# Optimization experiments

Measured on AMD Instinct MI355X. Metric: run time of the kernel, lower is better.

## Reference

```python
import jax, jax.numpy as jnp
import numpy as np

EMB = 1024
HEADS = 16
HEAD_DIM = EMB // HEADS
B, T = 2, 2048
EPS = 1e-5


def setup_inputs() -> dict:
    key = jax.random.key(0)
    ks = jax.random.split(key, 12)
    s_in = (1.0 / np.sqrt(EMB)).astype(np.float32)
    s_hid = (1.0 / np.sqrt(4 * EMB)).astype(np.float32)
    return {
        "x": jax.random.normal(ks[0], (B, T, EMB), jnp.float32),
        "Wq": jax.random.normal(ks[1], (HEADS, EMB, HEAD_DIM), jnp.float32) * s_in,
        "Wk": jax.random.normal(ks[2], (HEADS, EMB, HEAD_DIM), jnp.float32) * s_in,
        "Wv": jax.random.normal(ks[3], (HEADS, EMB, HEAD_DIM), jnp.float32) * s_in,
        "W1": jax.random.normal(ks[4], (EMB, 4 * EMB), jnp.float32) * s_in,
        "b1": jnp.zeros((4 * EMB,), jnp.float32),
        "W2": jax.random.normal(ks[5], (4 * EMB, EMB), jnp.float32) * s_hid,
        "b2": jnp.zeros((EMB,), jnp.float32),
        "g1": jnp.ones((EMB,), jnp.float32),
        "be1": jnp.zeros((EMB,), jnp.float32),
        "g2": jnp.ones((EMB,), jnp.float32),
        "be2": jnp.zeros((EMB,), jnp.float32),
    }


def _layernorm1d(x, gain, bias):
    # Faithful to source: normalize over dim 1 (sequence dim of [B,T,C]),
    # with UNBIASED variance (torch.var default).
    mean = jnp.mean(x, axis=1, keepdims=True)
    var = jnp.var(x, axis=1, keepdims=True, ddof=1)
    return gain * (x - mean) / jnp.sqrt(var + EPS) + bias


def _attention(x, Wq, Wk, Wv):
    Bq, Tq, C = x.shape
    q = jnp.einsum("btc,hcd->bhtd", x, Wq)
    k = jnp.einsum("btc,hcd->bhtd", x, Wk)
    v = jnp.einsum("btc,hcd->bhtd", x, Wv)
    # NOTE: scale uses input channel dim C (=emb_size), as in the source.
    wei = jnp.einsum("bhtd,bhsd->bhts", q, k) * (C ** -0.5)
    causal = jnp.tril(jnp.ones((Tq, Tq), bool))
    wei = jnp.where(causal, wei, -jnp.inf)
    wei = jax.nn.softmax(wei, axis=-1)
    out = jnp.einsum("bhts,bhsd->bhtd", wei, v)
    # concat over heads (dim=-1) == transpose + reshape
    return out.transpose(0, 2, 1, 3).reshape(Bq, Tq, -1)


def reference(x, Wq, Wk, Wv, W1, b1, W2, b2, g1, be1, g2, be2):
    x = x + _attention(_layernorm1d(x, g1, be1), Wq, Wk, Wv)
    h = _layernorm1d(x, g2, be2)
    h = jax.nn.relu(h @ W1 + b1) @ W2 + b2
    return x + h
```

## Files before the change

### kernel.cpp

```cpp
#include <hip/hip_runtime.h>


typedef __bf16 bf16x8 __attribute__((ext_vector_type(8)));
typedef float f32x4 __attribute__((ext_vector_type(4)));
typedef unsigned short u16;
typedef u16 u16x8 __attribute__((ext_vector_type(8)));
typedef u16 u16x4 __attribute__((ext_vector_type(4)));

#define MFMA16 __builtin_amdgcn_mfma_f32_16x16x32_bf16

__device__ __forceinline__ u16 f2bf(float f) {
  return __builtin_bit_cast(u16, (__bf16)f);
}
__device__ __forceinline__ float bf2f(u16 u) {
  return __builtin_bit_cast(float, (unsigned)u << 16);
}
__device__ __forceinline__ bf16x8 ldbf8(const u16* p) {
  return __builtin_bit_cast(bf16x8, *reinterpret_cast<const u16x8*>(p));
}
__device__ __forceinline__ void gll16(const void* g, void* l) {
  __builtin_amdgcn_global_load_lds((const __attribute__((address_space(1))) void*)g,
                                   (__attribute__((address_space(3))) void*)l, 16, 0, 0);
}
template <int N>
__device__ __forceinline__ void wait_vm() {
  if constexpr (N == 0)      asm volatile("s_waitcnt vmcnt(0)" ::: "memory");
  else if constexpr (N == 4) asm volatile("s_waitcnt vmcnt(4)" ::: "memory");
  else if constexpr (N == 6) asm volatile("s_waitcnt vmcnt(6)" ::: "memory");
  else if constexpr (N == 8) asm volatile("s_waitcnt vmcnt(8)" ::: "memory");
  else                       asm volatile("s_waitcnt vmcnt(16)" ::: "memory");
}
__device__ __forceinline__ void barrier_raw() {
  asm volatile("" ::: "memory");
  __builtin_amdgcn_s_barrier();
  asm volatile("" ::: "memory");
}
__device__ __forceinline__ int qb_off(int qb) {
  if (qb < 8)  return qb;
  if (qb < 16) return 8 + (qb - 8) * 2;
  if (qb < 24) return 24 + (qb - 16) * 3;
  return 48 + (qb - 24) * 4;
}

__global__ __launch_bounds__(256) void transpose_big(const float* __restrict__ in,
                                                     u16* __restrict__ out, int K, int N) {
  __shared__ float tile[64][65];
  const int k0 = blockIdx.x * 64, n0 = blockIdx.y * 64;
  const int c = threadIdx.x & 63, rg = threadIdx.x >> 6;
#pragma unroll
  for (int i = 0; i < 16; ++i) {
    int r = rg * 16 + i;
    tile[r][c] = in[(size_t)(k0 + r) * N + n0 + c];
  }
  __syncthreads();
#pragma unroll
  for (int i = 0; i < 16; ++i) {
    int nl = rg * 16 + i;
    out[(size_t)(n0 + nl) * K + k0 + c] = f2bf(tile[c][nl]);
  }
}

__global__ __launch_bounds__(256) void transpose_head3(const float* __restrict__ Wq,
                                                       const float* __restrict__ Wk,
                                                       const float* __restrict__ Wv,
                                                       u16* __restrict__ out, float scale) {
  __shared__ float tile[64][65];
  const int z = blockIdx.z;
  const float* W = z == 0 ? Wq : (z == 1 ? Wk : Wv);
  const float sc = z == 0 ? scale : 1.0f;
  const int k0 = blockIdx.x * 64, h = blockIdx.y;
  const float* in = W + (size_t)h * 1024 * 64;
  const int c = threadIdx.x & 63, rg = threadIdx.x >> 6;
#pragma unroll
  for (int i = 0; i < 16; ++i) {
    int r = rg * 16 + i;
    tile[r][c] = in[(size_t)(k0 + r) * 64 + c];
  }
  __syncthreads();
#pragma unroll
  for (int i = 0; i < 16; ++i) {
    int nl = rg * 16 + i;
    out[(size_t)(z * 1024 + h * 64 + nl) * 1024 + k0 + c] = f2bf(tile[c][nl] * sc);
  }
}

__global__ __launch_bounds__(256) void ln_partial(const float* __restrict__ x,
                                                  float2* __restrict__ part) {
  const int b = blockIdx.x >> 4, c0 = (blockIdx.x & 15) * 64;
  const int c = c0 + (threadIdx.x & 63), tg = threadIdx.x >> 6;
  const int t0 = blockIdx.y * 256 + tg * 64;
  float s = 0.f, sq = 0.f;
  const float* p = x + (size_t)(b * 2048 + t0) * 1024 + c;
#pragma unroll 8
  for (int i = 0; i < 64; ++i) {
    float v = p[(size_t)i * 1024];
    s += v; sq += v * v;
  }
  __shared__ float ss[256], sb[256];
  ss[threadIdx.x] = s; sb[threadIdx.x] = sq;
  __syncthreads();
  if (threadIdx.x < 64) {
    s  = ss[threadIdx.x] + ss[threadIdx.x + 64] + ss[threadIdx.x + 128] + ss[threadIdx.x + 192];
    sq = sb[threadIdx.x] + sb[threadIdx.x + 64] + sb[threadIdx.x + 128] + sb[threadIdx.x + 192];
    part[(size_t)(b * 1024 + c) * 8 + blockIdx.y] = make_float2(s, sq);
  }
}

__global__ __launch_bounds__(256) void ln_stats(const float2* __restrict__ part,
                                                float2* __restrict__ stats) {
  const int bc = blockIdx.x * 256 + threadIdx.x;
  float s = 0.f, sq = 0.f;
#pragma unroll
  for (int i = 0; i < 8; ++i) {
    float2 v = part[(size_t)bc * 8 + i];
    s += v.x; sq += v.y;
  }
  const float mean = s * (1.0f / 2048.0f);
  const float var = (sq - 2048.0f * mean * mean) * (1.0f / 2047.0f);
  stats[bc] = make_float2(mean, rsqrtf(var + 1e-5f));
}

__global__ __launch_bounds__(256) void ln_apply(const float* __restrict__ x,
                                                const float2* __restrict__ stats,
                                                const float* __restrict__ g,
                                                const float* __restrict__ be,
                                                u16* __restrict__ out) {
  const size_t flat = ((size_t)blockIdx.x * 256 + threadIdx.x) * 4;
  const int b = (int)(flat >> 21);
  const int c = (int)(flat & 1023);
  float4 xv = *reinterpret_cast<const float4*>(x + flat);
  float vs[4] = {xv.x, xv.y, xv.z, xv.w};
  u16x4 o;
#pragma unroll
  for (int j = 0; j < 4; ++j) {
    float2 st = stats[b * 1024 + c + j];
    o[j] = f2bf(g[c + j] * (vs[j] - st.x) * st.y + be[c + j]);
  }
  *reinterpret_cast<u16x4*>(out + flat) = o;
}

template <int WTN, int EPI, int MINW>
__global__ __launch_bounds__(256, MINW) void gemm_kernel(const u16* __restrict__ A,
                                                         const u16* __restrict__ Bt,
                                                         u16* __restrict__ outb,
                                                         float* __restrict__ outf,
                                                         const float* __restrict__ bias,
                                                         const float* __restrict__ resid,
                                                         int N, int K) {
  constexpr int BM = 128, BN = 2 * WTN;
  constexpr int NI = WTN / 16;
  constexpr int BCH = BN / 8;
  constexpr int LPW = (16 + BCH) / 4;
  __shared__ alignas(16) u16 sA[2][BM * 64];
  __shared__ alignas(16) u16 sB[2][BN * 64];
  const int gx = gridDim.x;
  const int nwg = gx * gridDim.y;
  int bid = blockIdx.y * gx + blockIdx.x;
  bid = (bid & 7) * (nwg >> 3) + (bid >> 3);
  const int n0 = (bid % gx) * BN, m0 = (bid / gx) * BM;
  const int tid = threadIdx.x, lane = tid & 63, wid = tid >> 6;
  const int wm = (wid >> 1) * 64, wn = (wid & 1) * WTN;
  const int lr = lane & 15, lg = lane >> 4;
  const int srow = lane >> 3;
  const int sgr = (lane & 7) ^ srow;
  const int x7 = lr & 7;
  f32x4 acc[4][NI] = {};

  auto stage = [&](int buf, int k0) {
#pragma unroll
    for (int i = 0; i < LPW; ++i) {
      const int c = wid * LPW + i;
      if (c < 16) {
        const int r = c * 8 + srow;
        gll16(A + (size_t)(m0 + r) * K + k0 + sgr * 8, &sA[buf][c * 512]);
      } else {
        const int r = (c - 16) * 8 + srow;
        gll16(Bt + (size_t)(n0 + r) * K + k0 + sgr * 8, &sB[buf][(c - 16) * 512]);
      }
    }
  };

  const int nsteps = K >> 6;
  stage(0, 0);
  int cur = 0;
  for (int t = 0; t < nsteps; ++t) {
    if (t + 1 < nsteps) {
      stage(cur ^ 1, (t + 1) * 64);
      wait_vm<LPW>();
    } else {
      wait_vm<0>();
    }
    barrier_raw();
    bf16x8 af[4][2], bfr[NI][2];
#pragma unroll
    for (int mi = 0; mi < 4; ++mi)
#pragma unroll
      for (int kk = 0; kk < 2; ++kk)
        af[mi][kk] = ldbf8(&sA[cur][(wm + mi * 16 + lr) * 64 + (((kk * 4 + lg) ^ x7) * 8)]);
#pragma unroll
    for (int ni = 0; ni < NI; ++ni)
#pragma unroll
      for (int kk = 0; kk < 2; ++kk)
        bfr[ni][kk] = ldbf8(&sB[cur][(wn + ni * 16 + lr) * 64 + (((kk * 4 + lg) ^ x7) * 8)]);
#pragma unroll
    for (int kk = 0; kk < 2; ++kk)
#pragma unroll
      for (int mi = 0; mi < 4; ++mi)
#pragma unroll
        for (int ni = 0; ni < NI; ++ni)
          acc[mi][ni] = MFMA16(af[mi][kk], bfr[ni][kk], acc[mi][ni], 0, 0, 0);
    barrier_raw();
    cur ^= 1;
  }

#pragma unroll
  for (int mi = 0; mi < 4; ++mi)
#pragma unroll
    for (int ni = 0; ni < NI; ++ni)
#pragma unroll
      for (int r = 0; r < 4; ++r) {
        const int row = m0 + wm + mi * 16 + lg * 4 + r;
        const int col = n0 + wn + ni * 16 + lr;
        float v = acc[mi][ni][r];
        if (EPI == 0) {
          outb[(size_t)row * N + col] = f2bf(v);
        } else if (EPI == 1) {
          v += bias[col];
          v = fmaxf(v, 0.f);
          outb[(size_t)row * N + col] = f2bf(v);
        } else {
          v += bias[col] + resid[(size_t)row * N + col];
          outf[(size_t)row * N + col] = v;
        }
      }
}

__global__ __launch_bounds__(256) void attn_partial(const u16* __restrict__ qk,
                                                    const u16* __restrict__ vt,
                                                    u16* __restrict__ Opart,
                                                    float2* __restrict__ ml) {
  const int xr = 79 - (int)blockIdx.x;
  int qb, ch, nc;
  if (xr < 8)       { qb = xr;                ch = 0;            nc = 1; }
  else if (xr < 24) { qb = 8 + ((xr - 8) >> 1);  ch = (xr - 8) & 1;  nc = 2; }
  else if (xr < 48) { qb = 16 + (xr - 24) / 3;   ch = (xr - 24) % 3; nc = 3; }
  else              { qb = 24 + ((xr - 48) >> 2); ch = (xr - 48) & 3; nc = 4; }
  const int nt_tot = qb + 1;
  const int t0 = (ch * nt_tot) / nc;
  const int t1 = ((ch + 1) * nt_tot) / nc;
  const int bh = blockIdx.y, b = bh >> 4, h = bh & 15;
  const int slot = bh * 80 + xr;
  const int q0 = qb * 64;
  const int tid = threadIdx.x, lane = tid & 63, w = tid >> 6;
  const int lr = lane & 15, lg = lane >> 4;
  __shared__ alignas(16) u16 sK[2][64 * 64];
  __shared__ alignas(16) u16 sV[2][64 * 64];
  __shared__ alignas(16) u16 sP[4][16 * 64];

  const size_t qrow = (size_t)(b * 2048 + q0 + w * 16 + lr) * 2048 + h * 64;
  const bf16x8 aq0 = ldbf8(qk + qrow + lg * 8);
  const bf16x8 aq1 = ldbf8(qk + qrow + 32 + lg * 8);

  float m_i[4], l_i[4];
  f32x4 acc[4];
#pragma unroll
  for (int r = 0; r < 4; ++r) { m_i[r] = -1e30f; l_i[r] = 0.f; }
#pragma unroll
  for (int dn = 0; dn < 4; ++dn) acc[dn] = f32x4{0.f, 0.f, 0.f, 0.f};

  auto stage = [&](int buf, int s0) {
#pragma unroll
    for (int i = 0; i < 2; ++i) {
      const int c = w * 2 + i;
      const int g = c * 64 + lane;
      const int row = g >> 3;
      const int cs = (g & 7) ^ (row & 7);
      gll16(qk + (size_t)(b * 2048 + s0 + row) * 2048 + 1024 + h * 64 + cs * 8,
            &sK[buf][c * 512]);
      gll16(vt + (size_t)(h * 64 + row) * 4096 + b * 2048 + s0 + cs * 8,
            &sV[buf][c * 512]);
    }
  };

  stage(0, t0 * 64);

  for (int t = t0; t < t1; ++t) {
    const int buf = (t - t0) & 1;
    if (t + 1 < t1) {
      stage(buf ^ 1, (t + 1) * 64);
      wait_vm<4>();
    } else {
      wait_vm<0>();
    }
    barrier_raw();

    const u16* Kb = sK[buf];
    const u16* Vb = sV[buf];
    f32x4 sf[4];
    __builtin_amdgcn_s_setprio(1);
#pragma unroll
    for (int sn = 0; sn < 4; ++sn) {
      const int row = sn * 16 + lr;
      const int x7 = lr & 7;
      bf16x8 k0f = ldbf8(&Kb[row * 64 + ((lg ^ x7) * 8)]);
      bf16x8 k1f = ldbf8(&Kb[row * 64 + (((4 + lg) ^ x7) * 8)]);
      f32x4 z = {0.f, 0.f, 0.f, 0.f};
      z = MFMA16(aq0, k0f, z, 0, 0, 0);
      z = MFMA16(aq1, k1f, z, 0, 0, 0);
      sf[sn] = z;
    }
    __builtin_amdgcn_s_setprio(0);

    if (t == nt_tot - 1) {
      const int qlb = w * 16 + lg * 4;
#pragma unroll
      for (int sn = 0; sn < 4; ++sn)
#pragma unroll
        for (int r = 0; r < 4; ++r)
          if (sn * 16 + lr > qlb + r) sf[sn][r] = -1e30f;
    }

    float pm[4];
    bool need = false;
#pragma unroll
    for (int r = 0; r < 4; ++r) {
      pm[r] = fmaxf(fmaxf(sf[0][r], sf[1][r]), fmaxf(sf[2][r], sf[3][r]));
      need = need || (pm[r] > m_i[r] + 8.f);
    }
    if (__any(need)) {
#pragma unroll
      for (int r = 0; r < 4; ++r) {
        float mx = pm[r];
        mx = fmaxf(mx, __shfl_xor(mx, 1, 16));
        mx = fmaxf(mx, __shfl_xor(mx, 2, 16));
        mx = fmaxf(mx, __shfl_xor(mx, 4, 16));
        mx = fmaxf(mx, __shfl_xor(mx, 8, 16));
        const float mnew = fmaxf(m_i[r], mx);
        const float al = exp2f(m_i[r] - mnew);
        l_i[r] *= al;
        acc[0][r] *= al; acc[1][r] *= al; acc[2][r] *= al; acc[3][r] *= al;
        m_i[r] = mnew;
      }
    }

    const int x7p = lr & 7;
#pragma unroll
    for (int r = 0; r < 4; ++r) {
      const float p0 = exp2f(sf[0][r] - m_i[r]), p1 = exp2f(sf[1][r] - m_i[r]);
      const float p2 = exp2f(sf[2][r] - m_i[r]), p3 = exp2f(sf[3][r] - m_i[r]);
      l_i[r] += (p0 + p1) + (p2 + p3);
      const int prow = lg * 4 + r;
      const int pb = prow * 64, px = prow & 7;
      sP[w][pb + (((lr >> 3) ^ px) * 8) + (lr & 7)]       = f2bf(p0);
      sP[w][pb + (((2 + (lr >> 3)) ^ px) * 8) + (lr & 7)] = f2bf(p1);
      sP[w][pb + (((4 + (lr >> 3)) ^ px) * 8) + (lr & 7)] = f2bf(p2);
      sP[w][pb + (((6 + (lr >> 3)) ^ px) * 8) + (lr & 7)] = f2bf(p3);
    }

    const bf16x8 pa0 = ldbf8(&sP[w][lr * 64 + ((lg ^ x7p) * 8)]);
    const bf16x8 pa1 = ldbf8(&sP[w][lr * 64 + (((4 + lg) ^ x7p) * 8)]);
    __builtin_amdgcn_s_setprio(1);
#pragma unroll
    for (int dn = 0; dn < 4; ++dn) {
      const int row = dn * 16 + lr;
      bf16x8 v0f = ldbf8(&Vb[row * 64 + ((lg ^ x7p) * 8)]);
      bf16x8 v1f = ldbf8(&Vb[row * 64 + (((4 + lg) ^ x7p) * 8)]);
      acc[dn] = MFMA16(pa0, v0f, acc[dn], 0, 0, 0);
      acc[dn] = MFMA16(pa1, v1f, acc[dn], 0, 0, 0);
    }
    __builtin_amdgcn_s_setprio(0);
    barrier_raw();
  }

  const int rbase = w * 16 + lg * 4;
#pragma unroll
  for (int r = 0; r < 4; ++r) {
    float ls = l_i[r];
    ls += __shfl_xor(ls, 1, 16);
    ls += __shfl_xor(ls, 2, 16);
    ls += __shfl_xor(ls, 4, 16);
    ls += __shfl_xor(ls, 8, 16);
    const int row = rbase + r;
    if (lr == 0) ml[(size_t)slot * 64 + row] = make_float2(m_i[r], ls);
#pragma unroll
    for (int dn = 0; dn < 4; ++dn)
      Opart[((size_t)slot * 64 + row) * 64 + dn * 16 + lr] = f2bf(acc[dn][r]);
  }
}

__global__ __launch_bounds__(256) void attn_merge(const u16* __restrict__ Opart,
                                                  const float2* __restrict__ ml,
                                                  const float* __restrict__ x,
                                                  float* __restrict__ x2) {
  const int qb = blockIdx.x, bh = blockIdx.y, b = bh >> 4, h = bh & 15;
  const int nc = (qb >> 3) + 1;
  const size_t slot0 = (size_t)bh * 80 + qb_off(qb);
  const int tid = threadIdx.x;
  const int row = tid >> 2, d0 = (tid & 3) * 16;

  float wgt[4];
  float mmax = -1e30f, lsum = 0.f;
  for (int i = 0; i < nc; ++i) {
    float2 v = ml[(slot0 + i) * 64 + row];
    wgt[i] = v.x;
    mmax = fmaxf(mmax, v.x);
  }
  for (int i = 0; i < nc; ++i) {
    float2 v = ml[(slot0 + i) * 64 + row];
    wgt[i] = exp2f(wgt[i] - mmax);
    lsum += wgt[i] * v.y;
  }
  const float inv = 1.0f / lsum;

#pragma unroll
  for (int half = 0; half < 2; ++half) {
    const int d = d0 + half * 8;
    float o[8] = {0.f, 0.f, 0.f, 0.f, 0.f, 0.f, 0.f, 0.f};
    for (int i = 0; i < nc; ++i) {
      u16x8 v = *reinterpret_cast<const u16x8*>(&Opart[((slot0 + i) * 64 + row) * 64 + d]);
#pragma unroll
      for (int jj = 0; jj < 8; ++jj) o[jj] += wgt[i] * bf2f(v[jj]);
    }
    const size_t idx = ((size_t)(b * 2048 + qb * 64 + row)) * 1024 + h * 64 + d;
    float4 x0 = *reinterpret_cast<const float4*>(x + idx);
    float4 x1 = *reinterpret_cast<const float4*>(x + idx + 4);
    float4 o0 = make_float4(x0.x + o[0] * inv, x0.y + o[1] * inv, x0.z + o[2] * inv, x0.w + o[3] * inv);
    float4 o1 = make_float4(x1.x + o[4] * inv, x1.y + o[5] * inv, x1.z + o[6] * inv, x1.w + o[7] * inv);
    *reinterpret_cast<float4*>(x2 + idx) = o0;
    *reinterpret_cast<float4*>(x2 + idx + 4) = o1;
  }
}

extern "C" void kernel_launch(void* const* d_in, const int* in_sizes, int n_in,
                              void* d_out, int out_size, void* d_ws, size_t ws_size,
                              hipStream_t stream) {
  const float* x   = (const float*)d_in[0];
  const float* Wq  = (const float*)d_in[1];
  const float* Wk  = (const float*)d_in[2];
  const float* Wv  = (const float*)d_in[3];
  const float* W1  = (const float*)d_in[4];
  const float* b1  = (const float*)d_in[5];
  const float* W2  = (const float*)d_in[6];
  const float* b2  = (const float*)d_in[7];
  const float* g1  = (const float*)d_in[8];
  const float* be1 = (const float*)d_in[9];
  const float* g2  = (const float*)d_in[10];
  const float* be2 = (const float*)d_in[11];
  float* out = (float*)d_out;

  char* ws = (char*)d_ws;
  size_t off = 0;
  auto alloc = [&](size_t bytes) { char* p = ws + off; off += (bytes + 255) & ~(size_t)255; return p; };
  u16*    qkb   = (u16*)alloc(4096ull * 2048 * 2);
  u16*    vtb   = (u16*)alloc(1024ull * 4096 * 2);
  (void)alloc(4096ull * 1024 * 2);
  u16*    h1    = qkb;
  float*  x2    = (float*)alloc(4096ull * 1024 * 4);
  u16*    hbuf  = (u16*)alloc(4096ull * 1024 * 2);
  u16*    wqkvt = (u16*)alloc(3072ull * 1024 * 2);
  u16*    w1t   = (u16*)alloc(4096ull * 1024 * 2);
  u16*    w2t   = (u16*)alloc(1024ull * 4096 * 2);
  float2* part  = (float2*)alloc(2048ull * 8 * 8);
  float2* stats = (float2*)alloc(2048ull * 8);
  u16*    Opart = (u16*)alloc(32ull * 80 * 64 * 64 * 2);
  float2* ml    = (float2*)alloc(32ull * 80 * 64 * 8);
  (void)ws_size; (void)in_sizes; (void)n_in; (void)out_size;

  const float SC = 0.03125f * 1.44269504088896341f;
  transpose_head3<<<dim3(16, 16, 3), 256, 0, stream>>>(Wq, Wk, Wv, wqkvt, SC);
  transpose_big<<<dim3(16, 64), 256, 0, stream>>>(W1, w1t, 1024, 4096);
  transpose_big<<<dim3(64, 16), 256, 0, stream>>>(W2, w2t, 4096, 1024);

  ln_partial<<<dim3(32, 8), 256, 0, stream>>>(x, part);
  ln_stats<<<8, 256, 0, stream>>>(part, stats);
  ln_apply<<<4096, 256, 0, stream>>>(x, stats, g1, be1, hbuf);

  gemm_kernel<64, 0, 2><<<dim3(16, 32), 256, 0, stream>>>(hbuf, wqkvt, qkb, nullptr, nullptr, nullptr, 2048, 1024);
  gemm_kernel<32, 0, 3><<<dim3(64, 8), 256, 0, stream>>>(wqkvt + 2048 * 1024, hbuf, vtb, nullptr, nullptr, nullptr, 4096, 1024);

  attn_partial<<<dim3(80, 32), 256, 0, stream>>>(qkb, vtb, Opart, ml);
  attn_merge<<<dim3(32, 32), 256, 0, stream>>>(Opart, ml, x, x2);

  ln_partial<<<dim3(32, 8), 256, 0, stream>>>(x2, part);
  ln_stats<<<8, 256, 0, stream>>>(part, stats);
  ln_apply<<<4096, 256, 0, stream>>>(x2, stats, g2, be2, hbuf);

  gemm_kernel<64, 1, 2><<<dim3(32, 32), 256, 0, stream>>>(hbuf, w1t, h1, nullptr, b1, nullptr, 4096, 1024);

  gemm_kernel<32, 2, 3><<<dim3(16, 32), 256, 0, stream>>>(h1, w2t, nullptr, out, b2, x2, 1024, 4096);
}
```

Before: 248.5 us.

## Fuse LN2 partial stats into attention merge, merge transposes, single-buffer attention

The attention merge kernel now reduces per-column sum and sum-of-squares over its 64-row tile and writes them as layernorm partials, removing the separate ln_partial pass over x2. The W1 and W2 transposes are combined into one launch. The attention kernel drops double-buffered K/V staging in favor of a single buffer with a full wait each tile, reducing LDS use but exposing load latency. The LN stats kernel is templated on the number of partials.

After: 237.4 us. 4.4% less time.

```diff
diff --git a/kernel.cpp b/kernel.cpp
--- a/kernel.cpp
+++ b/kernel.cpp
@@ -25,7 +25,6 @@
 template <int N>
 __device__ __forceinline__ void wait_vm() {
   if constexpr (N == 0)      asm volatile("s_waitcnt vmcnt(0)" ::: "memory");
-  else if constexpr (N == 4) asm volatile("s_waitcnt vmcnt(4)" ::: "memory");
   else if constexpr (N == 6) asm volatile("s_waitcnt vmcnt(6)" ::: "memory");
   else if constexpr (N == 8) asm volatile("s_waitcnt vmcnt(8)" ::: "memory");
   else                       asm volatile("s_waitcnt vmcnt(16)" ::: "memory");
@@ -42,10 +41,18 @@
   return 48 + (qb - 24) * 4;
 }
 
-__global__ __launch_bounds__(256) void transpose_big(const float* __restrict__ in,
-                                                     u16* __restrict__ out, int K, int N) {
+__global__ __launch_bounds__(256) void transpose_big2(const float* __restrict__ W1,
+                                                      const float* __restrict__ W2,
+                                                      u16* __restrict__ o1,
+                                                      u16* __restrict__ o2) {
   __shared__ float tile[64][65];
-  const int k0 = blockIdx.x * 64, n0 = blockIdx.y * 64;
+  int id = blockIdx.x;
+  const float* in;
+  u16* out;
+  int K, N, kb, nb;
+  if (id < 1024) { in = W1; out = o1; K = 1024; N = 4096; kb = id & 15; nb = id >> 4; }
+  else { id -= 1024; in = W2; out = o2; K = 4096; N = 1024; kb = id >> 4; nb = id & 15; }
+  const int k0 = kb * 64, n0 = nb * 64;
   const int c = threadIdx.x & 63, rg = threadIdx.x >> 6;
 #pragma unroll
   for (int i = 0; i < 16; ++i) {
@@ -106,13 +113,14 @@
   }
 }
 
+template <int NC>
 __global__ __launch_bounds__(256) void ln_stats(const float2* __restrict__ part,
                                                 float2* __restrict__ stats) {
   const int bc = blockIdx.x * 256 + threadIdx.x;
   float s = 0.f, sq = 0.f;
 #pragma unroll
-  for (int i = 0; i < 8; ++i) {
-    float2 v = part[(size_t)bc * 8 + i];
+  for (int i = 0; i < NC; ++i) {
+    float2 v = part[(size_t)bc * NC + i];
     s += v.x; sq += v.y;
   }
   const float mean = s * (1.0f / 2048.0f);
@@ -253,8 +261,8 @@
   const int q0 = qb * 64;
   const int tid = threadIdx.x, lane = tid & 63, w = tid >> 6;
   const int lr = lane & 15, lg = lane >> 4;
-  __shared__ alignas(16) u16 sK[2][64 * 64];
-  __shared__ alignas(16) u16 sV[2][64 * 64];
+  __shared__ alignas(16) u16 sK[64 * 64];
+  __shared__ alignas(16) u16 sV[64 * 64];
   __shared__ alignas(16) u16 sP[4][16 * 64];
 
   const size_t qrow = (size_t)(b * 2048 + q0 + w * 16 + lr) * 2048 + h * 64;
@@ -268,7 +276,7 @@
 #pragma unroll
   for (int dn = 0; dn < 4; ++dn) acc[dn] = f32x4{0.f, 0.f, 0.f, 0.f};
 
-  auto stage = [&](int buf, int s0) {
+  auto stage = [&](int s0) {
 #pragma unroll
     for (int i = 0; i < 2; ++i) {
       const int c = w * 2 + i;
@@ -276,34 +284,25 @@
       const int row = g >> 3;
       const int cs = (g & 7) ^ (row & 7);
       gll16(qk + (size_t)(b * 2048 + s0 + row) * 2048 + 1024 + h * 64 + cs * 8,
-            &sK[buf][c * 512]);
+            &sK[c * 512]);
       gll16(vt + (size_t)(h * 64 + row) * 4096 + b * 2048 + s0 + cs * 8,
-            &sV[buf][c * 512]);
+            &sV[c * 512]);
     }
   };
 
-  stage(0, t0 * 64);
-
   for (int t = t0; t < t1; ++t) {
-    const int buf = (t - t0) & 1;
-    if (t + 1 < t1) {
-      stage(buf ^ 1, (t + 1) * 64);
-      wait_vm<4>();
-    } else {
-      wait_vm<0>();
-    }
+    stage(t * 64);
+    wait_vm<0>();
     barrier_raw();
 
-    const u16* Kb = sK[buf];
-    const u16* Vb = sV[buf];
     f32x4 sf[4];
     __builtin_amdgcn_s_setprio(1);
 #pragma unroll
     for (int sn = 0; sn < 4; ++sn) {
       const int row = sn * 16 + lr;
       const int x7 = lr & 7;
-      bf16x8 k0f = ldbf8(&Kb[row * 64 + ((lg ^ x7) * 8)]);
-      bf16x8 k1f = ldbf8(&Kb[row * 64 + (((4 + lg) ^ x7) * 8)]);
+      bf16x8 k0f = ldbf8(&sK[row * 64 + ((lg ^ x7) * 8)]);
+      bf16x8 k1f = ldbf8(&sK[row * 64 + (((4 + lg) ^ x7) * 8)]);
       f32x4 z = {0.f, 0.f, 0.f, 0.f};
       z = MFMA16(aq0, k0f, z, 0, 0, 0);
       z = MFMA16(aq1, k1f, z, 0, 0, 0);
@@ -363,8 +362,8 @@
 #pragma unroll
     for (int dn = 0; dn < 4; ++dn) {
       const int row = dn * 16 + lr;
-      bf16x8 v0f = ldbf8(&Vb[row * 64 + ((lg ^ x7p) * 8)]);
-      bf16x8 v1f = ldbf8(&Vb[row * 64 + (((4 + lg) ^ x7p) * 8)]);
+      bf16x8 v0f = ldbf8(&sV[row * 64 + ((lg ^ x7p) * 8)]);
+      bf16x8 v1f = ldbf8(&sV[row * 64 + (((4 + lg) ^ x7p) * 8)]);
       acc[dn] = MFMA16(pa0, v0f, acc[dn], 0, 0, 0);
       acc[dn] = MFMA16(pa1, v1f, acc[dn], 0, 0, 0);
     }
@@ -388,15 +387,17 @@
   }
 }
 
-__global__ __launch_bounds__(256) void attn_merge(const u16* __restrict__ Opart,
-                                                  const float2* __restrict__ ml,
-                                                  const float* __restrict__ x,
-                                                  float* __restrict__ x2) {
+__global__ __launch_bounds__(256) void attn_merge_ln(const u16* __restrict__ Opart,
+                                                     const float2* __restrict__ ml,
+                                                     const float* __restrict__ x,
+                                                     float* __restrict__ x2,
+                                                     float2* __restrict__ part) {
   const int qb = blockIdx.x, bh = blockIdx.y, b = bh >> 4, h = bh & 15;
   const int nc = (qb >> 3) + 1;
   const size_t slot0 = (size_t)bh * 80 + qb_off(qb);
   const int tid = threadIdx.x;
   const int row = tid >> 2, d0 = (tid & 3) * 16;
+  __shared__ float red[64][65];
 
   float wgt[4];
   float mmax = -1e30f, lsum = 0.f;
@@ -428,6 +429,18 @@
     float4 o1 = make_float4(x1.x + o[4] * inv, x1.y + o[5] * inv, x1.z + o[6] * inv, x1.w + o[7] * inv);
     *reinterpret_cast<float4*>(x2 + idx) = o0;
     *reinterpret_cast<float4*>(x2 + idx + 4) = o1;
+    red[row][d + 0] = o0.x; red[row][d + 1] = o0.y; red[row][d + 2] = o0.z; red[row][d + 3] = o0.w;
+    red[row][d + 4] = o1.x; red[row][d + 5] = o1.y; red[row][d + 6] = o1.z; red[row][d + 7] = o1.w;
+  }
+  __syncthreads();
+  if (tid < 64) {
+    float s = 0.f, sq = 0.f;
+#pragma unroll 8
+    for (int t = 0; t < 64; ++t) {
+      float v = red[t][tid];
+      s += v; sq += v * v;
+    }
+    part[(size_t)(b * 1024 + h * 64 + tid) * 32 + qb] = make_float2(s, sq);
   }
 }
 
@@ -460,7 +473,7 @@
   u16*    wqkvt = (u16*)alloc(3072ull * 1024 * 2);
   u16*    w1t   = (u16*)alloc(4096ull * 1024 * 2);
   u16*    w2t   = (u16*)alloc(1024ull * 4096 * 2);
-  float2* part  = (float2*)alloc(2048ull * 8 * 8);
+  float2* part  = (float2*)alloc(2048ull * 32 * 8);
   float2* stats = (float2*)alloc(2048ull * 8);
   u16*    Opart = (u16*)alloc(32ull * 80 * 64 * 64 * 2);
   float2* ml    = (float2*)alloc(32ull * 80 * 64 * 8);
@@ -468,21 +481,19 @@
 
   const float SC = 0.03125f * 1.44269504088896341f;
   transpose_head3<<<dim3(16, 16, 3), 256, 0, stream>>>(Wq, Wk, Wv, wqkvt, SC);
-  transpose_big<<<dim3(16, 64), 256, 0, stream>>>(W1, w1t, 1024, 4096);
-  transpose_big<<<dim3(64, 16), 256, 0, stream>>>(W2, w2t, 4096, 1024);
+  transpose_big2<<<2048, 256, 0, stream>>>(W1, W2, w1t, w2t);
 
   ln_partial<<<dim3(32, 8), 256, 0, stream>>>(x, part);
-  ln_stats<<<8, 256, 0, stream>>>(part, stats);
+  ln_stats<8><<<8, 256, 0, stream>>>(part, stats);
   ln_apply<<<4096, 256, 0, stream>>>(x, stats, g1, be1, hbuf);
 
   gemm_kernel<64, 0, 2><<<dim3(16, 32), 256, 0, stream>>>(hbuf, wqkvt, qkb, nullptr, nullptr, nullptr, 2048, 1024);
   gemm_kernel<32, 0, 3><<<dim3(64, 8), 256, 0, stream>>>(wqkvt + 2048 * 1024, hbuf, vtb, nullptr, nullptr, nullptr, 4096, 1024);
 
   attn_partial<<<dim3(80, 32), 256, 0, stream>>>(qkb, vtb, Opart, ml);
-  attn_merge<<<dim3(32, 32), 256, 0, stream>>>(Opart, ml, x, x2);
-
-  ln_partial<<<dim3(32, 8), 256, 0, stream>>>(x2, part);
-  ln_stats<<<8, 256, 0, stream>>>(part, stats);
+  attn_merge_ln<<<dim3(32, 32), 256, 0, stream>>>(Opart, ml, x, x2, part);
+
+  ln_stats<32><<<8, 256, 0, stream>>>(part, stats);
   ln_apply<<<4096, 256, 0, stream>>>(x2, stats, g2, be2, hbuf);
 
   gemm_kernel<64, 1, 2><<<dim3(32, 32), 256, 0, stream>>>(hbuf, w1t, h1, nullptr, b1, nullptr, 4096, 1024);
```
